# Kernel optimization log

Hardware: AMD Instinct MI355X
Metric: run time of the kernel (lower is better)

The kernel has to match this reference:

```python
import jax, jax.numpy as jnp
import numpy as np

N_OBJ = 256   # number of RoIs/objects
C = 151       # num_obj_classes (Visual Genome)
H = 512       # hidden_dim == output_dim
T = 3         # time_step


def setup_inputs() -> dict:
    key = jax.random.key(0)
    ks = jax.random.split(key, 12)
    s = jnp.float32(0.02)

    def lin(k, out_dim, in_dim):
        k1, k2 = jax.random.split(k)
        w = jax.random.normal(k1, (out_dim, in_dim), jnp.float32) * s
        b = jax.random.normal(k2, (out_dim,), jnp.float32) * s
        return w, b

    inp = {}
    inp['input_ggnn'] = jax.random.normal(ks[0], (N_OBJ, H), jnp.float32)
    inp['matrix'] = jax.random.uniform(ks[1], (C, C), jnp.float32)
    for i, name in enumerate(['eq3_w', 'eq3_u', 'eq4_w', 'eq4_u', 'eq5_w', 'eq5_u']):
        in_dim = 2 * H if name.endswith('_w') else H
        w, b = lin(ks[2 + i], H, in_dim)
        inp['w_' + name] = w
        inp['b_' + name] = b
    w, b = lin(ks[8], H, 2 * H)
    inp['w_out'], inp['b_out'] = w, b
    w, b = lin(ks[9], C, C * H)
    inp['w_cls'], inp['b_cls'] = w, b
    return inp


def _ggnn_obj(input_ggnn, matrix,
              w_eq3_w, b_eq3_w, w_eq3_u, b_eq3_u,
              w_eq4_w, b_eq4_w, w_eq4_u, b_eq4_u,
              w_eq5_w, b_eq5_w, w_eq5_u, b_eq5_u,
              w_out, b_out, w_cls, b_cls):
    n = input_ggnn.shape[0]
    # hidden[i, c] = input_ggnn[i] for every class slot c  -> [N, C, H]
    hidden0 = jnp.broadcast_to(input_ggnn[:, None, :], (n, C, H))

    def step(hidden, _):
        hidden_sum = hidden.sum(axis=0)                # [C, H]
        x = hidden_sum[None, :, :] - hidden            # [N, C, H]
        # matrix.T @ x_i  and  matrix @ x_i, vectorized over N
        av1 = jnp.einsum('cd,nch->ndh', matrix, x)     # M^T propagation
        av2 = jnp.einsum('dc,nch->ndh', matrix, x)     # M propagation
        av = jnp.concatenate([av1, av2], axis=-1).reshape(n * C, 2 * H)
        h = hidden.reshape(n * C, H)
        zv = jax.nn.sigmoid(av @ w_eq3_w.T + b_eq3_w + h @ w_eq3_u.T + b_eq3_u)
        rv = jax.nn.sigmoid(av @ w_eq4_w.T + b_eq4_w + h @ w_eq4_u.T + b_eq4_u)
        hv = jnp.tanh(av @ w_eq5_w.T + b_eq5_w + (rv * h) @ w_eq5_u.T + b_eq5_u)
        h = (1.0 - zv) * h + zv * hv
        return h.reshape(n, C, H), None

    hidden, _ = jax.lax.scan(step, hidden0, None, length=T)

    inp_rep = hidden0.reshape(n * C, H)                # input repeated per class slot
    out = jnp.concatenate([hidden.reshape(n * C, H), inp_rep], axis=1)  # [N*C, 2H]
    out = jax.nn.relu(out @ w_out.T + b_out)           # [N*C, H]
    obj_dists = out.reshape(n, C * H) @ w_cls.T + b_cls  # [N, C]
    return obj_dists


def reference(input_ggnn, matrix,
              w_eq3_w, b_eq3_w, w_eq3_u, b_eq3_u,
              w_eq4_w, b_eq4_w, w_eq4_u, b_eq4_u,
              w_eq5_w, b_eq5_w, w_eq5_u, b_eq5_u,
              w_out, b_out, w_cls, b_cls):
    return _ggnn_obj(input_ggnn, matrix,
                     w_eq3_w, b_eq3_w, w_eq3_u, b_eq3_u,
                     w_eq4_w, b_eq4_w, w_eq4_u, b_eq4_u,
                     w_eq5_w, b_eq5_w, w_eq5_u, b_eq5_u,
                     w_out, b_out, w_cls, b_cls)
```

## Files before the change

kernel.cpp:

```cpp
#include <hip/hip_runtime.h>


#define C_     151
#define H_     512
#define NOBJ   256
#define NR     38656
#define NCH    64
#define CH     9664
#define CHP    9728
#define KPAD   160
#define KLDS   168
#define KA     2560
#define KV     3584
#define KB     2560

typedef _Float16 half8 __attribute__((ext_vector_type(8)));
typedef _Float16 half4 __attribute__((ext_vector_type(4)));
typedef float    f32x4 __attribute__((ext_vector_type(4)));

__device__ __forceinline__ float sigm(float x) { return 1.f / (1.f + expf(-x)); }

__device__ __forceinline__ void gload16(const void* g, void* l) {
    __builtin_amdgcn_global_load_lds(
        (const __attribute__((address_space(1))) void*)g,
        (__attribute__((address_space(3))) void*)l, 16, 0, 0);
}

__device__ __forceinline__ int kqswz(int s) {
    return 8 * (((s & 3) + 8 - ((s >> 2) & 3) - ((s >> 4) & 3)) & 3);
}
__device__ __forceinline__ int fraswz(int lane) {
    const int lb = lane & 15;
    return lb * 32 + 8 * (((lane >> 4) + lb + (lb >> 2)) & 3);
}

__device__ __forceinline__ half8 loadA8(const _Float16* p) { return *(const half8*)p; }
__device__ __forceinline__ half8 loadA8(const float* p) {
    f32x4 a = *(const f32x4*)p;
    f32x4 b = *(const f32x4*)(p + 4);
    half8 o;
    #pragma unroll
    for (int j = 0; j < 4; ++j) { o[j] = (_Float16)a[j]; o[4 + j] = (_Float16)b[j]; }
    return o;
}

template<int OP, typename AT, bool DUPK>
__global__ __launch_bounds__(256, 2)
void gemm_kernel(const AT* __restrict__ A, int lda,
                 const _Float16* __restrict__ B, int ldb,
                 void* __restrict__ Out, int ldo,
                 const float* __restrict__ bias,
                 const float* __restrict__ bias2,
                 int kchunk, int chunkStride)
{
    constexpr bool A16 = (sizeof(AT) == 2);
    __shared__ _Float16 sA[128 * 32];
    __shared__ _Float16 sB[128 * 32];
    const int tid  = threadIdx.x;
    const int lane = tid & 63;
    const int w    = tid >> 6;
    const int m0   = blockIdx.x * 128;
    const int n0   = blockIdx.y * 128;
    const int kbase = blockIdx.z * kchunk;

    const int s0 = tid, s1 = tid + 256;
    const AT* Ap0 = A + (size_t)(m0 + (s0 >> 2)) * lda + kqswz(s0);
    const AT* Ap1 = A + (size_t)(m0 + (s1 >> 2)) * lda + kqswz(s1);
    const _Float16* Bp0 = B + (size_t)(n0 + (s0 >> 2)) * ldb + kbase + kqswz(s0);
    const _Float16* Bp1 = B + (size_t)(n0 + (s1 >> 2)) * ldb + kbase + kqswz(s1);
    const int la0 = 8 * s0;
    const int la1 = 8 * s1;
    _Float16* lA0 = &sA[w * 512];
    _Float16* lA1 = &sA[2048 + w * 512];
    _Float16* lB0 = &sB[w * 512];
    _Float16* lB1 = &sB[2048 + w * 512];

    f32x4 acc[4][4];
    #pragma unroll
    for (int i = 0; i < 4; ++i)
        #pragma unroll
        for (int j = 0; j < 4; ++j)
            #pragma unroll
            for (int r = 0; r < 4; ++r) acc[i][j][r] = 0.f;

    const int mrow = (w >> 1) * 64;
    const int ncol = (w & 1) * 64;
    const int fra  = fraswz(lane);

    for (int k0 = 0; k0 < kchunk; k0 += 32) {
        int kA;
        if (DUPK) kA = (k0 < 2048) ? k0 : ((k0 < 3072) ? k0 - 2048 : k0 - 1024);
        else      kA = kbase + k0;
        if constexpr (A16) {
            __syncthreads();
            gload16(Ap0 + kA, lA0);
            gload16(Ap1 + kA, lA1);
            gload16(Bp0 + k0, lB0);
            gload16(Bp1 + k0, lB1);
            __syncthreads();
        } else {
            half8 va0 = loadA8(Ap0 + kA);
            half8 va1 = loadA8(Ap1 + kA);
            half8 vb0 = *(const half8*)(Bp0 + k0);
            half8 vb1 = *(const half8*)(Bp1 + k0);
            __syncthreads();
            *(half8*)&sA[la0] = va0;
            *(half8*)&sA[la1] = va1;
            *(half8*)&sB[la0] = vb0;
            *(half8*)&sB[la1] = vb1;
            __syncthreads();
        }
        half8 af[4], bf[4];
        #pragma unroll
        for (int i = 0; i < 4; ++i)
            af[i] = *(const half8*)&sA[(mrow + i * 16) * 32 + fra];
        #pragma unroll
        for (int i = 0; i < 4; ++i)
            bf[i] = *(const half8*)&sB[(ncol + i * 16) * 32 + fra];
        #pragma unroll
        for (int mi = 0; mi < 4; ++mi)
            #pragma unroll
            for (int ni = 0; ni < 4; ++ni)
                acc[mi][ni] = __builtin_amdgcn_mfma_f32_16x16x32_f16(af[mi], bf[ni], acc[mi][ni], 0, 0, 0);
    }

    const size_t zoff = (size_t)blockIdx.z * (size_t)chunkStride;
    #pragma unroll
    for (int mi = 0; mi < 4; ++mi) {
        #pragma unroll
        for (int ni = 0; ni < 4; ++ni) {
            #pragma unroll
            for (int r = 0; r < 4; ++r) {
                const int row = m0 + mrow + mi * 16 + (lane >> 4) * 4 + r;
                const int col = n0 + ncol + ni * 16 + (lane & 15);
                float v = acc[mi][ni][r];
                const size_t o = zoff + (size_t)row * ldo + col;
                if (OP == 0) {
                    ((float*)Out)[o] = v;
                } else if (OP == 1) {
                    ((_Float16*)Out)[o] = (_Float16)v;
                } else {
                    const unsigned n = (unsigned)row / 151u;
                    v += bias[col] + bias2[n * 512u + col];
                    v = v > 0.f ? v : 0.f;
                    ((_Float16*)Out)[o] = (_Float16)v;
                }
            }
        }
    }
}

__global__ __launch_bounds__(512, 2)
void gemm256(const _Float16* __restrict__ A, const _Float16* __restrict__ B,
             _Float16* __restrict__ Out)
{
    constexpr int LDA = KA;
    constexpr int LDB = KB;
    constexpr int LDO = 1536;
    constexpr int NT  = KV / 64;
    __shared__ _Float16 lds[2][32768];

    const int tid  = threadIdx.x;
    const int lane = tid & 63;
    const int w    = tid >> 6;
    const int m0   = blockIdx.x * 256;
    const int n0   = blockIdx.y * 256;

    const int tr  = tid >> 3;
    const int swz = ((tid & 7) ^ (tr & 7)) << 3;
    const _Float16* Ap = A + (size_t)(m0 + tr) * LDA + swz;
    const _Float16* Bp = B + (size_t)(n0 + tr) * LDB + swz;
    const int ldsbase = w << 9;

    auto stage = [&](int buf, int kAb, int kBb) {
        _Float16* L = &lds[buf][0];
        #pragma unroll
        for (int h = 0; h < 2; ++h) {
            #pragma unroll
            for (int r = 0; r < 2; ++r) {
                const int ro = h * 128 + r * 64;
                gload16(Ap + (size_t)ro * LDA + kAb, L + h * 8192 + r * 4096 + ldsbase);
                gload16(Bp + (size_t)ro * LDB + kBb, L + 16384 + h * 8192 + r * 4096 + ldsbase);
            }
        }
    };

    const int lb = lane & 15;
    const int lq = lane >> 4;
    auto frag = [&](const _Float16* base, int row0, int ks) -> half8 {
        const int row = row0 + lb;
        const int kg  = ks * 4 + lq;
        return *(const half8*)&base[row * 64 + ((kg ^ (row & 7)) << 3)];
    };

    const int wm = (w >> 2) * 128;
    const int wn = (w & 3) * 64;

    f32x4 acc[8][4];
    #pragma unroll
    for (int i = 0; i < 8; ++i)
        #pragma unroll
        for (int j = 0; j < 4; ++j)
            #pragma unroll
            for (int r = 0; r < 4; ++r) acc[i][j][r] = 0.f;

    half8 a[4][2], b0[2][2], b1[2][2];

#define QUAD(MQ, NQ, BB) do {                                                   \
    __builtin_amdgcn_s_barrier();                                               \
    asm volatile("s_waitcnt lgkmcnt(0)" ::: "memory");                          \
    __builtin_amdgcn_s_setprio(1);                                              \
    _Pragma("unroll")                                                           \
    for (int i = 0; i < 4; ++i) {                                               \
        _Pragma("unroll")                                                       \
        for (int j = 0; j < 2; ++j) {                                           \
            _Pragma("unroll")                                                   \
            for (int ks = 0; ks < 2; ++ks)                                      \
                acc[(MQ) * 4 + i][(NQ) * 2 + j] =                               \
                    __builtin_amdgcn_mfma_f32_16x16x32_f16(                     \
                        a[i][ks], BB[j][ks],                                    \
                        acc[(MQ) * 4 + i][(NQ) * 2 + j], 0, 0, 0);              \
        }                                                                       \
    }                                                                           \
    __builtin_amdgcn_s_setprio(0);                                              \
    __builtin_amdgcn_s_barrier();                                               \
} while (0)

    stage(0, 0, 0);
    asm volatile("s_waitcnt vmcnt(0)" ::: "memory");
    __builtin_amdgcn_s_barrier();

    for (int t = 0; t < NT; ++t) {
        const _Float16* sA = &lds[t & 1][0];
        const _Float16* sB = &lds[t & 1][16384];

        #pragma unroll
        for (int i = 0; i < 4; ++i) {
            a[i][0] = frag(sA, wm + i * 16, 0);
            a[i][1] = frag(sA, wm + i * 16, 1);
        }
        #pragma unroll
        for (int j = 0; j < 2; ++j) {
            b0[j][0] = frag(sB, wn + j * 16, 0);
            b0[j][1] = frag(sB, wn + j * 16, 1);
        }
        if (t + 1 < NT) {
            const int kk  = (t + 1) * 64;
            const int kAb = (kk < 2048) ? kk : ((kk < 3072) ? kk - 2048 : kk - 1024);
            const int kBb = (kk < 1024) ? kk : kk - 1024;
            stage((t + 1) & 1, kAb, kBb);
        }
        QUAD(0, 0, b0);

        #pragma unroll
        for (int j = 0; j < 2; ++j) {
            b1[j][0] = frag(sB, wn + 32 + j * 16, 0);
            b1[j][1] = frag(sB, wn + 32 + j * 16, 1);
        }
        QUAD(0, 1, b1);

        #pragma unroll
        for (int i = 0; i < 4; ++i) {
            a[i][0] = frag(sA, wm + 64 + i * 16, 0);
            a[i][1] = frag(sA, wm + 64 + i * 16, 1);
        }
        QUAD(1, 1, b1);

        asm volatile("s_waitcnt vmcnt(0)" ::: "memory");
        QUAD(1, 0, b0);
    }
#undef QUAD

    #pragma unroll
    for (int mi = 0; mi < 8; ++mi) {
        #pragma unroll
        for (int ni = 0; ni < 4; ++ni) {
            #pragma unroll
            for (int r = 0; r < 4; ++r) {
                const int row = m0 + wm + mi * 16 + (lane >> 4) * 4 + r;
                const int col = n0 + wn + ni * 16 + (lane & 15);
                Out[(size_t)row * LDO + col] = (_Float16)acc[mi][ni][r];
            }
        }
    }
}

__global__ __launch_bounds__(256, 2)
void mix_kernel(const float* __restrict__ hid, const float* __restrict__ S,
                const _Float16* __restrict__ MTh, const _Float16* __restrict__ MTl,
                const _Float16* __restrict__ Mrh, const _Float16* __restrict__ Mrl,
                _Float16* __restrict__ AVH, int cbase)
{
    __shared__ _Float16 sxh[64 * KLDS];
    __shared__ _Float16 sxl[64 * KLDS];
    const int n  = blockIdx.x;
    const int h0 = blockIdx.y * 64;
    const int tid = threadIdx.x;

    #pragma unroll
    for (int i = 0; i < 5; ++i) {
        const int s  = tid + 256 * i;
        const int c  = s >> 3;
        const int hg = s & 7;
        half8 oh, ol;
        if (c < C_) {
            const float* hp = &hid[(size_t)(cbase + n * C_ + c) * H_ + h0 + hg * 8];
            const float* sp = &S[c * H_ + h0 + hg * 8];
            half8 hh;
            #pragma unroll
            for (int j = 0; j < 8; ++j) {
                const float hv = hp[j];
                const float x = sp[j] - hv;
                const _Float16 hi = (_Float16)x;
                oh[j] = hi;
                ol[j] = (_Float16)(x - (float)hi);
                hh[j] = (_Float16)hv;
            }
            *(half8*)&AVH[(size_t)(n * C_ + c) * KA + 2048 + h0 + hg * 8] = hh;
        } else {
            #pragma unroll
            for (int j = 0; j < 8; ++j) { oh[j] = (_Float16)0.f; ol[j] = (_Float16)0.f; }
        }
        #pragma unroll
        for (int j = 0; j < 8; ++j) {
            sxh[(hg * 8 + j) * KLDS + c] = oh[j];
            sxl[(hg * 8 + j) * KLDS + c] = ol[j];
        }
    }
    __syncthreads();

    const int lane = tid & 63;
    const int w    = tid >> 6;
    const _Float16* Mhi = (w >> 1) ? Mrh : MTh;
    const _Float16* Mlo = (w >> 1) ? Mrl : MTl;
    const int hb = (w & 1) * 32;

    f32x4 acc[10][2];
    #pragma unroll
    for (int i = 0; i < 10; ++i)
        #pragma unroll
        for (int j = 0; j < 2; ++j)
            #pragma unroll
            for (int r = 0; r < 4; ++r) acc[i][j][r] = 0.f;

    #pragma unroll
    for (int pass = 0; pass < 3; ++pass) {
        const _Float16* Ma = (pass == 2) ? Mlo : Mhi;
        const _Float16* X  = (pass == 1) ? sxl : sxh;
        #pragma unroll
        for (int kk = 0; kk < 5; ++kk) {
            const int k0 = kk * 32;
            half8 bf[2];
            #pragma unroll
            for (int ht = 0; ht < 2; ++ht)
                bf[ht] = *(const half8*)&X[(hb + ht * 16 + (lane & 15)) * KLDS + k0 + 8 * (lane >> 4)];
            #pragma unroll
            for (int dt = 0; dt < 10; ++dt) {
                half8 af = *(const half8*)&Ma[(dt * 16 + (lane & 15)) * KPAD + k0 + 8 * (lane >> 4)];
                acc[dt][0] = __builtin_amdgcn_mfma_f32_16x16x32_f16(af, bf[0], acc[dt][0], 0, 0, 0);
                acc[dt][1] = __builtin_amdgcn_mfma_f32_16x16x32_f16(af, bf[1], acc[dt][1], 0, 0, 0);
            }
        }
    }

    const int mixoff = (w >> 1) * 512;
    #pragma unroll
    for (int dt = 0; dt < 10; ++dt) {
        #pragma unroll
        for (int ht = 0; ht < 2; ++ht) {
            #pragma unroll
            for (int r = 0; r < 4; ++r) {
                const int d = dt * 16 + (lane >> 4) * 4 + r;
                if (d < C_) {
                    const int h = h0 + hb + ht * 16 + (lane & 15);
                    const float v = acc[dt][ht][r];
                    const _Float16 hi = (_Float16)v;
                    const _Float16 lo = (_Float16)(v - (float)hi);
                    _Float16* rowp = AVH + (size_t)(n * C_ + d) * KA + mixoff + h;
                    rowp[0]    = hi;
                    rowp[1024] = lo;
                }
            }
        }
    }
}


__global__ void k_sreduce(const float* __restrict__ hid, float* __restrict__ Stmp)
{
    const int c  = blockIdx.x;
    const int g  = blockIdx.y;
    const int hw = threadIdx.x;
    const float* p = hid + (size_t)c * H_ + hw * 8;
    float s[8];
    #pragma unroll
    for (int j = 0; j < 8; ++j) s[j] = 0.f;
    const size_t stride = (size_t)C_ * H_;
    for (int n = g * 32; n < g * 32 + 32; ++n) {
        f32x4 a = *(const f32x4*)(p + (size_t)n * stride);
        f32x4 b = *(const f32x4*)(p + (size_t)n * stride + 4);
        #pragma unroll
        for (int j = 0; j < 4; ++j) { s[j] += a[j]; s[4 + j] += b[j]; }
    }
    float* o = Stmp + (size_t)g * (C_ * H_) + c * H_ + hw * 8;
    *(f32x4*)o       = f32x4{s[0], s[1], s[2], s[3]};
    *(f32x4*)(o + 4) = f32x4{s[4], s[5], s[6], s[7]};
}

__global__ void k_sfold(const float* __restrict__ Stmp, float* __restrict__ S)
{
    const int idx = blockIdx.x * 256 + threadIdx.x;
    float s = 0.f;
    #pragma unroll
    for (int g = 0; g < 8; ++g) s += Stmp[(size_t)g * (C_ * H_) + idx];
    S[idx] = s;
}

__global__ void k_ew1(_Float16* __restrict__ pre, const float* __restrict__ hid,
                      const float* __restrict__ bz, const float* __restrict__ br, int cbase)
{
    const int idx = blockIdx.x * 256 + threadIdx.x;
    const unsigned r = idx >> 7;
    const int o4 = (idx & 127) << 2;
    const size_t base = (size_t)r * 1536;
    half4 zp = *(const half4*)&pre[base + o4];
    half4 rp = *(const half4*)&pre[base + 512 + o4];
    f32x4 hd = *(const f32x4*)&hid[(size_t)(cbase + r) * H_ + o4];
    f32x4 bz4 = *(const f32x4*)&bz[o4];
    f32x4 br4 = *(const f32x4*)&br[o4];
    half4 zs, rh;
    #pragma unroll
    for (int j = 0; j < 4; ++j) {
        float z = sigm((float)zp[j] + bz4[j]);
        float rr = sigm((float)rp[j] + br4[j]);
        zs[j] = (_Float16)z;
        rh[j] = (_Float16)(rr * hd[j]);
    }
    *(half4*)&pre[base + o4] = zs;
    *(half4*)&pre[base + 512 + o4] = rh;
}

__global__ void k_ew2(const _Float16* __restrict__ pre, const _Float16* __restrict__ p5a,
                      const _Float16* __restrict__ p5b,
                      float* __restrict__ hid, const float* __restrict__ b5, int cbase)
{
    const int idx = blockIdx.x * 256 + threadIdx.x;
    const unsigned r = idx >> 7;
    const int o4 = (idx & 127) << 2;
    const size_t base = (size_t)r * 1536;
    half4 w5 = *(const half4*)&pre[base + 1024 + o4];
    half4 pa = *(const half4*)&p5a[(size_t)r * H_ + o4];
    half4 pb = *(const half4*)&p5b[(size_t)r * H_ + o4];
    half4 zz = *(const half4*)&pre[base + o4];
    f32x4 hd = *(const f32x4*)&hid[(size_t)(cbase + r) * H_ + o4];
    f32x4 b54 = *(const f32x4*)&b5[o4];
    #pragma unroll
    for (int j = 0; j < 4; ++j) {
        float t = tanhf((float)w5[j] + (float)pa[j] + (float)pb[j] + b54[j]);
        float z = (float)zz[j];
        hd[j] = (1.f - z) * hd[j] + z * t;
    }
    *(f32x4*)&hid[(size_t)(cbase + r) * H_ + o4] = hd;
}


__global__ void prep_wbig(const float* w3w, const float* w3u,
                          const float* w4w, const float* w4u,
                          const float* w5w, const float* w5u,
                          _Float16* __restrict__ Wbig)
{
    const int idx = blockIdx.x * 256 + threadIdx.x;
    const int op = idx / KB;
    const int j = idx - op * KB;
    const int g = op >> 9, o = op & 511;
    const float* ww = (g == 0) ? w3w : (g == 1) ? w4w : w5w;
    const float* wu = (g == 0) ? w3u : (g == 1) ? w4u : w5u;
    _Float16 out;
    if (j < 1024) {
        out = (_Float16)ww[o * 1024 + j];
    } else if (j < 2048) {
        const float v = ww[o * 1024 + (j - 1024)];
        const _Float16 hi = (_Float16)v;
        out = (_Float16)(v - (float)hi);
    } else {
        out = (g < 2) ? (_Float16)wu[o * 512 + (j - 2048)] : (_Float16)0.f;
    }
    Wbig[idx] = out;
}

__global__ void prep_m(const float* __restrict__ matrix,
                       _Float16* __restrict__ MTh, _Float16* __restrict__ MTl,
                       _Float16* __restrict__ Mrh, _Float16* __restrict__ Mrl)
{
    const int idx = blockIdx.x * 256 + threadIdx.x;
    const int d = idx / KPAD, c = idx - d * KPAD;
    float vT = 0.f, vR = 0.f;
    if (d < C_ && c < C_) { vT = matrix[c * C_ + d]; vR = matrix[d * C_ + c]; }
    const _Float16 th = (_Float16)vT;
    const _Float16 rh = (_Float16)vR;
    MTh[idx] = th; MTl[idx] = (_Float16)(vT - (float)th);
    Mrh[idx] = rh; Mrl[idx] = (_Float16)(vR - (float)rh);
}

__global__ void prep_wout(const float* __restrict__ wout,
                          _Float16* __restrict__ WL, _Float16* __restrict__ WR)
{
    const int idx = blockIdx.x * 256 + threadIdx.x;
    const int o = idx >> 9, j = idx & 511;
    WL[idx] = (_Float16)wout[o * 1024 + j];
    WR[idx] = (_Float16)wout[o * 1024 + 512 + j];
}

__global__ void prep_wcls(const float* __restrict__ wcls, _Float16* __restrict__ w16)
{
    const int k = blockIdx.x * 256 + threadIdx.x;
    const int d = blockIdx.y;
    w16[(size_t)d * (C_ * H_) + k] = (_Float16)wcls[(size_t)d * (C_ * H_) + k];
}

__global__ void k_cast(const float* __restrict__ src, _Float16* __restrict__ dst, int n)
{
    const int i = blockIdx.x * 256 + threadIdx.x;
    if (i < n) dst[i] = (_Float16)src[i];
}

__global__ void prep_bias(const float* b3w, const float* b3u, const float* b4w,
                          const float* b4u, const float* b5w, const float* b5u,
                          float* bz, float* br, float* b5)
{
    const int i = threadIdx.x;
    bz[i] = b3w[i] + b3u[i];
    br[i] = b4w[i] + b4u[i];
    b5[i] = b5w[i] + b5u[i];
}

__global__ void prep_hid(const float* __restrict__ input, float* __restrict__ hid)
{
    const int idx = blockIdx.x * 256 + threadIdx.x;
    const unsigned row = idx >> 7;
    const int h4 = (idx & 127) << 2;
    const unsigned n = row / 151u;
    f32x4 v = *(const f32x4*)&input[(size_t)n * H_ + h4];
    *(f32x4*)&hid[(size_t)row * H_ + h4] = v;
}

__global__ void k_reduce(const float* __restrict__ partial, const float* __restrict__ bcls,
                         float* __restrict__ out)
{
    const int idx = blockIdx.x * 256 + threadIdx.x;
    const unsigned n = (unsigned)idx / 151u;
    const unsigned d = (unsigned)idx - n * 151u;
    float s = 0.f;
    for (int z = 0; z < C_; ++z)
        s += partial[(size_t)z * (NOBJ * 256) + n * 256 + d];
    out[idx] = s + bcls[d];
}


extern "C" void kernel_launch(void* const* d_in, const int* in_sizes, int n_in,
                              void* d_out, int out_size, void* d_ws, size_t ws_size,
                              hipStream_t stream)
{
    const float* input  = (const float*)d_in[0];
    const float* matrix = (const float*)d_in[1];
    const float* w3w = (const float*)d_in[2];
    const float* b3w = (const float*)d_in[3];
    const float* w3u = (const float*)d_in[4];
    const float* b3u = (const float*)d_in[5];
    const float* w4w = (const float*)d_in[6];
    const float* b4w = (const float*)d_in[7];
    const float* w4u = (const float*)d_in[8];
    const float* b4u = (const float*)d_in[9];
    const float* w5w = (const float*)d_in[10];
    const float* b5w = (const float*)d_in[11];
    const float* w5u = (const float*)d_in[12];
    const float* b5u = (const float*)d_in[13];
    const float* wout = (const float*)d_in[14];
    const float* bout = (const float*)d_in[15];
    const float* wcls = (const float*)d_in[16];
    const float* bcls = (const float*)d_in[17];
    float* obj = (float*)d_out;

    char* ws = (char*)d_ws;
    size_t off = 0;
    auto take = [&](size_t bytes) -> char* {
        off = (off + 255) & ~(size_t)255;
        char* p = ws + off;
        off += bytes;
        return p;
    };

    _Float16* Wbig  = (_Float16*)take((size_t)1536 * KB * 2);
    _Float16* MTh   = (_Float16*)take((size_t)KPAD * KPAD * 2);
    _Float16* MTl   = (_Float16*)take((size_t)KPAD * KPAD * 2);
    _Float16* Mrh   = (_Float16*)take((size_t)KPAD * KPAD * 2);
    _Float16* Mrl   = (_Float16*)take((size_t)KPAD * KPAD * 2);
    _Float16* W5u16 = (_Float16*)take((size_t)512 * 512 * 2);
    _Float16* WL16  = (_Float16*)take((size_t)512 * 512 * 2);
    _Float16* WR16  = (_Float16*)take((size_t)512 * 512 * 2);
    _Float16* in16  = (_Float16*)take((size_t)256 * 512 * 2);
    float*    bz    = (float*)take(512 * 4);
    float*    br    = (float*)take(512 * 4);
    float*    b5    = (float*)take(512 * 4);
    float*    Stmp  = (float*)take((size_t)8 * C_ * H_ * 4);
    float*    S32   = (float*)take((size_t)C_ * H_ * 4);
    float*    base  = (float*)take((size_t)256 * 512 * 4);
    float*    hid32 = (float*)take((size_t)NR * H_ * 4);
    _Float16* AVH   = (_Float16*)take((size_t)CHP * KA * 2);
    _Float16* prec  = (_Float16*)take((size_t)CHP * 1536 * 2);
    _Float16* p5u = AVH;
    _Float16* OUT16 = AVH;
    _Float16* Wcls16 = (_Float16*)hid32;
    float* partial = (float*)((char*)hid32 + (size_t)NOBJ * C_ * H_ * 2);

    (void)in_sizes; (void)n_in; (void)out_size; (void)ws_size;

    prep_wbig<<<dim3((1536 * KB) / 256), 256, 0, stream>>>(w3w, w3u, w4w, w4u, w5w, w5u, Wbig);
    prep_m<<<dim3((KPAD * KPAD) / 256), 256, 0, stream>>>(matrix, MTh, MTl, Mrh, Mrl);
    k_cast<<<dim3((512 * 512) / 256), 256, 0, stream>>>(w5u, W5u16, 512 * 512);
    prep_wout<<<dim3((512 * 512) / 256), 256, 0, stream>>>(wout, WL16, WR16);
    k_cast<<<dim3((256 * 512) / 256), 256, 0, stream>>>(input, in16, 256 * 512);
    prep_bias<<<dim3(1), 512, 0, stream>>>(b3w, b3u, b4w, b4u, b5w, b5u, bz, br, b5);
    prep_hid<<<dim3((NR * 128) / 256), 256, 0, stream>>>(input, hid32);
    gemm_kernel<0, _Float16, false><<<dim3(2, 4, 1), 256, 0, stream>>>(
        in16, 512, WR16, 512, base, 512, nullptr, nullptr, 512, 0);

    for (int t = 0; t < 3; ++t) {
        k_sreduce<<<dim3(C_, 8), 64, 0, stream>>>(hid32, Stmp);
        k_sfold<<<dim3((C_ * H_) / 256), 256, 0, stream>>>(Stmp, S32);
        for (int cc = 0; cc < 4; ++cc) {
            const int cbase = cc * CH;
            mix_kernel<<<dim3(NCH, 8), 256, 0, stream>>>(
                hid32, S32, MTh, MTl, Mrh, Mrl, AVH, cbase);
            gemm256<<<dim3(CHP / 256, 1536 / 256, 1), 512, 0, stream>>>(
                AVH, Wbig, prec);
            k_ew1<<<dim3((CH * 128) / 256), 256, 0, stream>>>(prec, hid32, bz, br, cbase);
            gemm_kernel<1, _Float16, false><<<dim3(CHP / 128, 4, 2), 256, 0, stream>>>(
                prec + 512, 1536, W5u16, 512, p5u, 512, nullptr, nullptr, 256, CHP * 512);
            k_ew2<<<dim3((CH * 128) / 256), 256, 0, stream>>>(
                prec, p5u, p5u + (size_t)CHP * 512, hid32, b5, cbase);
        }
    }

    gemm_kernel<2, float, false><<<dim3(NR / 128, 512 / 128, 1), 256, 0, stream>>>(
        hid32, 512, WL16, 512, OUT16, 512, bout, base, 512, 0);

    prep_wcls<<<dim3((C_ * H_) / 256, C_), 256, 0, stream>>>(wcls, Wcls16);
    gemm_kernel<0, _Float16, false><<<dim3(NOBJ / 128, 256 / 128, C_), 256, 0, stream>>>(
        OUT16, C_ * H_, Wcls16, C_ * H_, partial, 256, nullptr, nullptr, 512, NOBJ * 256);
    k_reduce<<<dim3(NR / 256), 256, 0, stream>>>(partial, bcls, obj);
}
```

Baseline: 2.597 ms.

## Software-pipeline LDS fragment loads across MFMA phases and remap blocks per XCD

Restructures the gemm256 main loop so that LDS fragment reads for the next phase, including the next k-tile's A-low and B fragments, are issued before the current phase's MFMAs run. Each phase now uses a single barrier instead of two, so LDS latency can overlap with matrix math. It also remaps the linear workgroup id so that consecutive tiles land on the same XCD, which should improve L2 reuse of the A and B panels. The cost is more live fragment registers (four fragment sets instead of three), and the remap hardcodes a 29/28 split that assumes a specific grid size.

```diff
diff --git a/kernel.cpp b/kernel.cpp
--- a/kernel.cpp
+++ b/kernel.cpp
@@ -163,8 +163,13 @@
     const int tid  = threadIdx.x;
     const int lane = tid & 63;
     const int w    = tid >> 6;
-    const int m0   = blockIdx.x * 256;
-    const int n0   = blockIdx.y * 256;
+
+    const int lin  = blockIdx.y * gridDim.x + blockIdx.x;
+    const int xcd  = lin & 7;
+    const int sub  = lin >> 3;
+    const int wgid = (xcd < 4 ? xcd * 29 : 4 * 29 + (xcd - 4) * 28) + sub;
+    const int m0   = (wgid / 6) * 256;
+    const int n0   = (wgid % 6) * 256;
 
     const int tr  = tid >> 3;
     const int swz = ((tid & 7) ^ (tr & 7)) << 3;
@@ -204,11 +209,20 @@
             #pragma unroll
             for (int r = 0; r < 4; ++r) acc[i][j][r] = 0.f;
 
-    half8 a[4][2], b0[2][2], b1[2][2];
-
-#define QUAD(MQ, NQ, BB) do {                                                   \
+    half8 aL[4][2], aH[4][2], bA[2][2], bB[2][2];
+
+#define SYNC_LG() do {                                                          \
+    asm volatile("s_waitcnt lgkmcnt(0)" ::: "memory");                          \
     __builtin_amdgcn_s_barrier();                                               \
+    __builtin_amdgcn_sched_barrier(0);                                          \
+} while (0)
+#define SYNC_LGVM() do {                                                        \
     asm volatile("s_waitcnt lgkmcnt(0)" ::: "memory");                          \
+    asm volatile("s_waitcnt vmcnt(0)" ::: "memory");                            \
+    __builtin_amdgcn_s_barrier();                                               \
+    __builtin_amdgcn_sched_barrier(0);                                          \
+} while (0)
+#define PHASE_MFMA(AF, BF, MO, NO) do {                                         \
     __builtin_amdgcn_s_setprio(1);                                              \
     _Pragma("unroll")                                                           \
     for (int i = 0; i < 4; ++i) {                                               \
@@ -216,60 +230,76 @@
         for (int j = 0; j < 2; ++j) {                                           \
             _Pragma("unroll")                                                   \
             for (int ks = 0; ks < 2; ++ks)                                      \
-                acc[(MQ) * 4 + i][(NQ) * 2 + j] =                               \
+                acc[(MO) + i][(NO) + j] =                                       \
                     __builtin_amdgcn_mfma_f32_16x16x32_f16(                     \
-                        a[i][ks], BB[j][ks],                                    \
-                        acc[(MQ) * 4 + i][(NQ) * 2 + j], 0, 0, 0);              \
+                        AF[i][ks], BF[j][ks], acc[(MO) + i][(NO) + j], 0, 0, 0);\
         }                                                                       \
     }                                                                           \
     __builtin_amdgcn_s_setprio(0);                                              \
-    __builtin_amdgcn_s_barrier();                                               \
 } while (0)
 
     stage(0, 0, 0);
     asm volatile("s_waitcnt vmcnt(0)" ::: "memory");
     __builtin_amdgcn_s_barrier();
+    __builtin_amdgcn_sched_barrier(0);
+    #pragma unroll
+    for (int i = 0; i < 4; ++i) {
+        aL[i][0] = frag(&lds[0][0], wm + i * 16, 0);
+        aL[i][1] = frag(&lds[0][0], wm + i * 16, 1);
+    }
+    #pragma unroll
+    for (int j = 0; j < 2; ++j) {
+        bA[j][0] = frag(&lds[0][16384], wn + j * 16, 0);
+        bA[j][1] = frag(&lds[0][16384], wn + j * 16, 1);
+    }
 
     for (int t = 0; t < NT; ++t) {
-        const _Float16* sA = &lds[t & 1][0];
-        const _Float16* sB = &lds[t & 1][16384];
-
-        #pragma unroll
-        for (int i = 0; i < 4; ++i) {
-            a[i][0] = frag(sA, wm + i * 16, 0);
-            a[i][1] = frag(sA, wm + i * 16, 1);
-        }
-        #pragma unroll
-        for (int j = 0; j < 2; ++j) {
-            b0[j][0] = frag(sB, wn + j * 16, 0);
-            b0[j][1] = frag(sB, wn + j * 16, 1);
-        }
+        const _Float16* sA  = &lds[t & 1][0];
+        const _Float16* sB  = &lds[t & 1][16384];
+        const _Float16* sAn = &lds[(t + 1) & 1][0];
+        const _Float16* sBn = &lds[(t + 1) & 1][16384];
+
+        SYNC_LG();
         if (t + 1 < NT) {
             const int kk  = (t + 1) * 64;
             const int kAb = (kk < 2048) ? kk : ((kk < 3072) ? kk - 2048 : kk - 1024);
             const int kBb = (kk < 1024) ? kk : kk - 1024;
             stage((t + 1) & 1, kAb, kBb);
         }
-        QUAD(0, 0, b0);
-
         #pragma unroll
         for (int j = 0; j < 2; ++j) {
-            b1[j][0] = frag(sB, wn + 32 + j * 16, 0);
-            b1[j][1] = frag(sB, wn + 32 + j * 16, 1);
-        }
-        QUAD(0, 1, b1);
-
+            bB[j][0] = frag(sB, wn + 32 + j * 16, 0);
+            bB[j][1] = frag(sB, wn + 32 + j * 16, 1);
+        }
+        PHASE_MFMA(aL, bA, 0, 0);
+
+        SYNC_LG();
         #pragma unroll
         for (int i = 0; i < 4; ++i) {
-            a[i][0] = frag(sA, wm + 64 + i * 16, 0);
-            a[i][1] = frag(sA, wm + 64 + i * 16, 1);
-        }
-        QUAD(1, 1, b1);
-
-        asm volatile("s_waitcnt vmcnt(0)" ::: "memory");
-        QUAD(1, 0, b0);
-    }
-#undef QUAD
+            aH[i][0] = frag(sA, wm + 64 + i * 16, 0);
+            aH[i][1] = frag(sA, wm + 64 + i * 16, 1);
+        }
+        PHASE_MFMA(aL, bB, 0, 2);
+
+        SYNC_LGVM();
+        #pragma unroll
+        for (int i = 0; i < 4; ++i) {
+            aL[i][0] = frag(sAn, wm + i * 16, 0);
+            aL[i][1] = frag(sAn, wm + i * 16, 1);
+        }
+        PHASE_MFMA(aH, bA, 4, 0);
+
+        SYNC_LG();
+        #pragma unroll
+        for (int j = 0; j < 2; ++j) {
+            bA[j][0] = frag(sBn, wn + j * 16, 0);
+            bA[j][1] = frag(sBn, wn + j * 16, 1);
+        }
+        PHASE_MFMA(aH, bB, 4, 2);
+    }
+#undef SYNC_LG
+#undef SYNC_LGVM
+#undef PHASE_MFMA
 
     #pragma unroll
     for (int mi = 0; mi < 8; ++mi) {
```

After: 2.542 ms. -2.1%, faster.
